# Optimization experiments

Hardware: AMD Instinct MI355X
Metric: run time of the kernel (lower is better)

The kernel has to match this reference:

```python
import jax, jax.numpy as jnp
import numpy as np
import math

B, S, D, H = 2, 2048, 1024, 16
DK = D // H


def setup_inputs() -> dict:
    key = jax.random.key(0)
    ks = jax.random.split(key, 14)
    inp = {
        "query": jax.random.normal(ks[0], (B, S, D), dtype=jnp.float32),
        "key": jax.random.normal(ks[1], (B, S, D), dtype=jnp.float32),
        "value": jax.random.normal(ks[2], (B, S, D), dtype=jnp.float32),
        "group_prob": jax.random.uniform(ks[3], (B, S, S), dtype=jnp.float32),
        "mask": jax.random.randint(ks[4], (B, S), 0, 2, dtype=jnp.int32),
    }
    scale = 0.02
    inp["Wq"] = jax.random.normal(ks[5], (D, D), dtype=jnp.float32) * scale
    inp["bq"] = jnp.zeros((D,), dtype=jnp.float32)
    inp["Wk"] = jax.random.normal(ks[6], (D, D), dtype=jnp.float32) * scale
    inp["bk"] = jnp.zeros((D,), dtype=jnp.float32)
    inp["Wv"] = jax.random.normal(ks[7], (D, D), dtype=jnp.float32) * scale
    inp["bv"] = jnp.zeros((D,), dtype=jnp.float32)
    inp["Wo"] = jax.random.normal(ks[8], (D, D), dtype=jnp.float32) * scale
    inp["bo"] = jnp.zeros((D,), dtype=jnp.float32)
    return inp


def reference(query, key, value, group_prob, mask, Wq, bq, Wk, bk, Wv, bv, Wo, bo):
    b, s, d = query.shape
    # project and split heads: [B,S,D] -> [B,H,S,DK]
    def proj(x, W, bias):
        return (x @ W.T + bias).reshape(b, s, H, DK).transpose(0, 2, 1, 3)

    q = proj(query, Wq, bq)
    k = proj(key, Wk, bk)
    v = proj(value, Wv, bv)

    scores = jnp.einsum("bhqd,bhkd->bhqk", q, k) / math.sqrt(DK)  # [B,H,S,S]

    # combined mask: padding-row mask OR diagonal (always attend to self)
    eye = jnp.eye(s, dtype=jnp.int32)
    combined = mask[:, None, None, :] | eye[None, None, :, :]  # [B,1,S,S]
    scores = jnp.where(combined == 0, jnp.float32(-1e9), scores)

    p_attn = jax.nn.softmax(scores, axis=-1)
    p_attn = p_attn * group_prob[:, None, :, :]  # post-softmax group scaling

    x = jnp.einsum("bhqk,bhkd->bhqd", p_attn, v)  # [B,H,S,DK]
    x = x.transpose(0, 2, 1, 3).reshape(b, s, d)
    return x @ Wo.T + bo
```

## Files before the change

### kernel.cpp

```cpp
#include <hip/hip_runtime.h>
#include <hip/hip_bf16.h>
#include <stdint.h>

typedef __bf16 bf16x8 __attribute__((ext_vector_type(8)));
typedef float f32x4 __attribute__((ext_vector_type(4)));

#define QSCALE 0.1803368801111244f

__device__ __forceinline__ void gld16(const void* g, void* l) {
  __builtin_amdgcn_global_load_lds(
      (__attribute__((address_space(1))) void*)(uintptr_t)(g),
      (__attribute__((address_space(3))) void*)(l), 16, 0, 0);
}

struct CastArgs {
  const float* src[7];
  __bf16* dst[7];
  int n[7];
};

__global__ __launch_bounds__(256) void cast_bf16_kernel(CastArgs a) {
  const int t = blockIdx.y;
  const int i = (blockIdx.x * 256 + threadIdx.x) * 8;
  if (i >= a.n[t]) return;
  const float4* s = (const float4*)(a.src[t] + i);
  float4 v0 = s[0], v1 = s[1];
  bf16x8 o;
  o[0] = (__bf16)v0.x; o[1] = (__bf16)v0.y; o[2] = (__bf16)v0.z; o[3] = (__bf16)v0.w;
  o[4] = (__bf16)v1.x; o[5] = (__bf16)v1.y; o[6] = (__bf16)v1.z; o[7] = (__bf16)v1.w;
  *(bf16x8*)(a.dst[t] + i) = o;
}

struct QkvArgs {
  const __bf16* A[3];
  const __bf16* B[3];
  const float* bias[3];
  __bf16* out[3];
};

__global__ __launch_bounds__(256) void qkv_gemm(QkvArgs args) {
  __shared__ __align__(16) __bf16 As[128 * 32];
  __shared__ __align__(16) __bf16 Bs[128 * 32];
  const int tid = threadIdx.x;
  const int z = blockIdx.y;
  const int bx = blockIdx.x;
  const int m0 = (z < 2 ? (bx >> 3) : (bx & 7)) * 128;
  const int n0 = (z < 2 ? (bx & 7) : (bx >> 3)) * 128;
  const __bf16* A = args.A[z];
  const __bf16* B = args.B[z];
  const float* bias = args.bias[z];
  __bf16* out = args.out[z];
  const float scale = (z == 0) ? QSCALE : 1.0f;

  const int lane = tid & 63, wid = tid >> 6;
  const int wm = (wid & 1) * 64, wn = (wid >> 1) * 64;
  const int l16 = lane & 15, quad = lane >> 4;

  const int sc = (tid & 3) ^ ((tid >> 2) & 3);
  const __bf16* ga = A + (size_t)(m0 + (tid >> 2)) * 1024 + sc * 8;
  const __bf16* gb = B + (size_t)(n0 + (tid >> 2)) * 1024 + sc * 8;
  char* lA = (char*)As + tid * 16;
  char* lB = (char*)Bs + tid * 16;
  const int a_off = (wm + l16) * 64 + ((quad ^ (l16 & 3)) * 16);
  const int b_off = (wn + l16) * 64 + ((quad ^ (l16 & 3)) * 16);

  f32x4 acc[4][4] = {};

  for (int k0 = 0; k0 < 1024; k0 += 32) {
    __syncthreads();
    gld16(ga + k0, lA);
    gld16(ga + k0 + 64 * 1024, lA + 4096);
    gld16(gb + k0, lB);
    gld16(gb + k0 + 64 * 1024, lB + 4096);
    __syncthreads();
    bf16x8 af[4], bfr[4];
#pragma unroll
    for (int mi = 0; mi < 4; ++mi)
      af[mi] = *(const bf16x8*)((const char*)As + a_off + mi * 1024);
#pragma unroll
    for (int ni = 0; ni < 4; ++ni)
      bfr[ni] = *(const bf16x8*)((const char*)Bs + b_off + ni * 1024);
#pragma unroll
    for (int mi = 0; mi < 4; ++mi)
#pragma unroll
      for (int ni = 0; ni < 4; ++ni)
        acc[mi][ni] = __builtin_amdgcn_mfma_f32_16x16x32_bf16(af[mi], bfr[ni],
                                                              acc[mi][ni], 0, 0, 0);
  }

  if (z < 2) {
#pragma unroll
    for (int ni = 0; ni < 4; ++ni) {
      const int col = n0 + wn + ni * 16 + l16;
      const int h = col >> 6, dk = col & 63;
      const float bb = bias[col];
#pragma unroll
      for (int mi = 0; mi < 4; ++mi)
#pragma unroll
        for (int r = 0; r < 4; ++r) {
          const int row = m0 + wm + mi * 16 + quad * 4 + r;
          const int b = row >> 11, s = row & 2047;
          out[((size_t)(b * 16 + h) * 2048 + s) * 64 + dk] =
              (__bf16)((acc[mi][ni][r] + bb) * scale);
        }
    }
  } else {
#pragma unroll
    for (int mi = 0; mi < 4; ++mi)
#pragma unroll
      for (int r = 0; r < 4; ++r) {
        const int rowm = m0 + wm + mi * 16 + quad * 4 + r;
        const int h = rowm >> 6, dk = rowm & 63;
        const float bb = bias[rowm];
#pragma unroll
        for (int ni = 0; ni < 4; ++ni) {
          const int coln = n0 + wn + ni * 16 + l16;
          const int b = coln >> 11, s = coln & 2047;
          out[((size_t)(b * 16 + h) * 64 + dk) * 2048 + s] =
              (__bf16)(acc[mi][ni][r] + bb);
        }
      }
  }
}

__global__ __launch_bounds__(256) void gemm_out(const __bf16* __restrict__ A,
                                                const __bf16* __restrict__ B,
                                                const float* __restrict__ bias,
                                                float* __restrict__ out) {
  __shared__ __align__(16) __bf16 As[128 * 32];
  __shared__ __align__(16) __bf16 Bs[128 * 32];
  const int tid = threadIdx.x;
  const int m0 = blockIdx.y * 128;
  const int n0 = blockIdx.x * 128;
  const int lane = tid & 63, wid = tid >> 6;
  const int wm = (wid & 1) * 64, wn = (wid >> 1) * 64;
  const int l16 = lane & 15, quad = lane >> 4;

  const int sc = (tid & 3) ^ ((tid >> 2) & 3);
  const __bf16* ga = A + (size_t)(m0 + (tid >> 2)) * 1024 + sc * 8;
  const __bf16* gb = B + (size_t)(n0 + (tid >> 2)) * 1024 + sc * 8;
  char* lA = (char*)As + tid * 16;
  char* lB = (char*)Bs + tid * 16;
  const int a_off = (wm + l16) * 64 + ((quad ^ (l16 & 3)) * 16);
  const int b_off = (wn + l16) * 64 + ((quad ^ (l16 & 3)) * 16);

  f32x4 acc[4][4] = {};

  for (int k0 = 0; k0 < 1024; k0 += 32) {
    __syncthreads();
    gld16(ga + k0, lA);
    gld16(ga + k0 + 64 * 1024, lA + 4096);
    gld16(gb + k0, lB);
    gld16(gb + k0 + 64 * 1024, lB + 4096);
    __syncthreads();
    bf16x8 af[4], bfr[4];
#pragma unroll
    for (int mi = 0; mi < 4; ++mi)
      af[mi] = *(const bf16x8*)((const char*)As + a_off + mi * 1024);
#pragma unroll
    for (int ni = 0; ni < 4; ++ni)
      bfr[ni] = *(const bf16x8*)((const char*)Bs + b_off + ni * 1024);
#pragma unroll
    for (int mi = 0; mi < 4; ++mi)
#pragma unroll
      for (int ni = 0; ni < 4; ++ni)
        acc[mi][ni] = __builtin_amdgcn_mfma_f32_16x16x32_bf16(af[mi], bfr[ni],
                                                              acc[mi][ni], 0, 0, 0);
  }

#pragma unroll
  for (int ni = 0; ni < 4; ++ni) {
    const int col = n0 + wn + ni * 16 + l16;
    const float bb = bias[col];
#pragma unroll
    for (int mi = 0; mi < 4; ++mi)
#pragma unroll
      for (int r = 0; r < 4; ++r) {
        const int row = m0 + wm + mi * 16 + quad * 4 + r;
        out[(size_t)row * 1024 + col] = acc[mi][ni][r] + bb;
      }
  }
}

__global__ __launch_bounds__(256) void attn_kernel(
    const __bf16* __restrict__ Qh, const __bf16* __restrict__ Kh,
    const __bf16* __restrict__ Vt, const float* __restrict__ gprob,
    const int* __restrict__ maskp, __bf16* __restrict__ xb) {
  __shared__ __align__(16) __bf16 Qs[64 * 64];
  __shared__ __align__(16) __bf16 Ks[2][64 * 64];
  __shared__ __align__(16) __bf16 Vs[2][64 * 64];
  __shared__ __align__(16) __bf16 Ps[4][16 * 64];
  __shared__ unsigned long long mbits[32];

  const int tid = threadIdx.x;
  const int qt = blockIdx.x, bh = blockIdx.y;
  const int b = bh >> 4, h = bh & 15;
  const int q0 = qt * 64;
  const int lane = tid & 63, wid = tid >> 6, l16 = lane & 15, quad = lane >> 4;
  const size_t head_off = (size_t)bh * (2048 * 64);

  const int srow = tid >> 3;
  const int sc8 = (tid & 7) ^ (srow & 7);
  const int fxor = (l16 & 7);

  const __bf16* gk0 = Kh + head_off + (size_t)srow * 64 + sc8 * 8;
  const __bf16* gv0 = Vt + head_off + (size_t)srow * 2048 + sc8 * 8;

  {
    const __bf16* gq = Qh + head_off + (size_t)(q0 + srow) * 64 + sc8 * 8;
    gld16(gq, (char*)Qs + tid * 16);
    gld16(gq + 32 * 64, (char*)Qs + 4096 + tid * 16);
    gld16(gk0, (char*)Ks + tid * 16);
    gld16(gk0 + 2048, (char*)Ks + 4096 + tid * 16);
    gld16(gv0, (char*)Vs + tid * 16);
    gld16(gv0 + 32 * 2048, (char*)Vs + 4096 + tid * 16);
  }
  {
    const int* mr = maskp + b * 2048;
#pragma unroll
    for (int t = 0; t < 8; ++t) {
      const int kt2 = wid * 8 + t;
      const int mv = mr[kt2 * 64 + lane];
      const unsigned long long bal = __ballot(mv != 0);
      if (lane == 0) mbits[kt2] = bal;
    }
  }
  __syncthreads();
  bf16x8 aq[2];
  aq[0] = *(const bf16x8*)((const char*)Qs + (wid * 16 + l16) * 128 +
                           ((quad ^ fxor) * 16));
  aq[1] = *(const bf16x8*)((const char*)Qs + (wid * 16 + l16) * 128 +
                           (((4 + quad) ^ fxor) * 16));

  f32x4 o[4] = {};
  float lp[4] = {0.f, 0.f, 0.f, 0.f};
  int irow[4];
#pragma unroll
  for (int r = 0; r < 4; ++r) irow[r] = q0 + wid * 16 + quad * 4 + r;

  const float* gpl = gprob + (size_t)b * 2048 * 2048 +
                     (size_t)(q0 + wid * 16 + l16) * 2048 + quad * 8;
  float4 g0 = *(const float4*)(gpl);
  float4 g1 = *(const float4*)(gpl + 4);
  float4 g2 = *(const float4*)(gpl + 32);
  float4 g3 = *(const float4*)(gpl + 36);

  for (int kt = 0; kt < 32; ++kt) {
    const int cur = kt & 1;
    float4 gn0, gn1, gn2, gn3;
    if (kt < 31) {
      const int nb = cur ^ 1;
      gld16(gk0 + (kt + 1) * 4096, (char*)Ks + nb * 8192 + tid * 16);
      gld16(gk0 + (kt + 1) * 4096 + 2048, (char*)Ks + nb * 8192 + 4096 + tid * 16);
      gld16(gv0 + (kt + 1) * 64, (char*)Vs + nb * 8192 + tid * 16);
      gld16(gv0 + (kt + 1) * 64 + 32 * 2048, (char*)Vs + nb * 8192 + 4096 + tid * 16);
      const float* gn = gpl + (kt + 1) * 64;
      gn0 = *(const float4*)(gn);
      gn1 = *(const float4*)(gn + 4);
      gn2 = *(const float4*)(gn + 32);
      gn3 = *(const float4*)(gn + 36);
    }

    const unsigned long long sh = mbits[kt] >> l16;
    const uint32_t shlo = (uint32_t)sh, shhi = (uint32_t)(sh >> 32);
    const bool mk[4] = {(shlo & 1) != 0, (shlo & 0x10000u) != 0,
                        (shhi & 1) != 0, (shhi & 0x10000u) != 0};

    f32x4 sc[4] = {};
#pragma unroll
    for (int kh = 0; kh < 2; ++kh)
#pragma unroll
      for (int ni = 0; ni < 4; ++ni) {
        bf16x8 bk = *(const bf16x8*)((const char*)Ks + cur * 8192 +
                                     (ni * 16 + l16) * 128 +
                                     (((kh * 4 + quad) ^ fxor) * 16));
        sc[ni] = __builtin_amdgcn_mfma_f32_16x16x32_bf16(aq[kh], bk, sc[ni], 0, 0, 0);
      }

    float pw[4][4];
    if (kt != qt) {
#pragma unroll
      for (int ni = 0; ni < 4; ++ni)
#pragma unroll
        for (int r = 0; r < 4; ++r) {
          const float e = __builtin_exp2f(sc[ni][r]);
          const float p = mk[ni] ? e : 0.f;
          lp[r] += p;
          pw[ni][r] = p;
        }
    } else {
#pragma unroll
      for (int ni = 0; ni < 4; ++ni)
#pragma unroll
        for (int r = 0; r < 4; ++r) {
          const float e = __builtin_exp2f(sc[ni][r]);
          const bool diag = (ni == wid) && (l16 == quad * 4 + r);
          const float p = (mk[ni] || diag) ? e : 0.f;
          lp[r] += p;
          pw[ni][r] = p;
        }
    }

#pragma unroll
    for (int ni = 0; ni < 4; ++ni)
#pragma unroll
      for (int r = 0; r < 4; ++r) {
        const int prow = quad * 4 + r;
        const int pchunk = (ni * 2 + (l16 >> 3)) ^ (prow & 7);
        *(__bf16*)((char*)&Ps[wid][0] + prow * 128 + pchunk * 16 + (l16 & 7) * 2) =
            (__bf16)pw[ni][r];
      }
    asm volatile("s_waitcnt lgkmcnt(0)" ::: "memory");

    const float gfl[16] = {g0.x, g0.y, g0.z, g0.w, g1.x, g1.y, g1.z, g1.w,
                           g2.x, g2.y, g2.z, g2.w, g3.x, g3.y, g3.z, g3.w};
#pragma unroll
    for (int kh = 0; kh < 2; ++kh) {
      bf16x8 ap = *(const bf16x8*)((const char*)&Ps[wid][0] + l16 * 128 +
                                   (((kh * 4 + quad) ^ fxor) * 16));
      bf16x8 apg;
#pragma unroll
      for (int j = 0; j < 8; ++j)
        apg[j] = (__bf16)((float)ap[j] * gfl[kh * 8 + j]);
#pragma unroll
      for (int ni = 0; ni < 4; ++ni) {
        bf16x8 bv = *(const bf16x8*)((const char*)Vs + cur * 8192 +
                                     (ni * 16 + l16) * 128 +
                                     (((kh * 4 + quad) ^ fxor) * 16));
        o[ni] = __builtin_amdgcn_mfma_f32_16x16x32_bf16(apg, bv, o[ni], 0, 0, 0);
      }
    }

    if (kt < 31) { g0 = gn0; g1 = gn1; g2 = gn2; g3 = gn3; }
    __syncthreads();
  }

#pragma unroll
  for (int r = 0; r < 4; ++r) {
    lp[r] += __shfl_xor(lp[r], 1);
    lp[r] += __shfl_xor(lp[r], 2);
    lp[r] += __shfl_xor(lp[r], 4);
    lp[r] += __shfl_xor(lp[r], 8);
    lp[r] = 1.f / lp[r];
  }
#pragma unroll
  for (int ni = 0; ni < 4; ++ni) {
    const int dk = ni * 16 + l16;
#pragma unroll
    for (int r = 0; r < 4; ++r) {
      const float val = o[ni][r] * lp[r];
      xb[((size_t)(b * 2048 + irow[r])) * 1024 + h * 64 + dk] = (__bf16)val;
    }
  }
}

extern "C" void kernel_launch(void* const* d_in, const int* in_sizes, int n_in,
                              void* d_out, int out_size, void* d_ws, size_t ws_size,
                              hipStream_t stream) {
  const float* query = (const float*)d_in[0];
  const float* key_  = (const float*)d_in[1];
  const float* value = (const float*)d_in[2];
  const float* gprob = (const float*)d_in[3];
  const int*   maskp = (const int*)d_in[4];
  const float* Wq = (const float*)d_in[5];
  const float* bq = (const float*)d_in[6];
  const float* Wk = (const float*)d_in[7];
  const float* bk = (const float*)d_in[8];
  const float* Wv = (const float*)d_in[9];
  const float* bv = (const float*)d_in[10];
  const float* Wo = (const float*)d_in[11];
  const float* bo = (const float*)d_in[12];

  char* ws = (char*)d_ws;
  const size_t MB = 1 << 20;
  __bf16* qb  = (__bf16*)(ws + 0 * MB);
  __bf16* kb  = (__bf16*)(ws + 8 * MB);
  __bf16* vb  = (__bf16*)(ws + 16 * MB);
  __bf16* Wqb = (__bf16*)(ws + 24 * MB);
  __bf16* Wkb = (__bf16*)(ws + 26 * MB);
  __bf16* Wvb = (__bf16*)(ws + 28 * MB);
  __bf16* Wob = (__bf16*)(ws + 30 * MB);
  __bf16* Qh  = (__bf16*)(ws + 32 * MB);
  __bf16* Kh  = (__bf16*)(ws + 40 * MB);
  __bf16* Vt  = (__bf16*)(ws + 48 * MB);
  __bf16* xb  = (__bf16*)(ws + 56 * MB);

  CastArgs ca;
  ca.src[0] = query; ca.dst[0] = qb;  ca.n[0] = 4194304;
  ca.src[1] = key_;  ca.dst[1] = kb;  ca.n[1] = 4194304;
  ca.src[2] = value; ca.dst[2] = vb;  ca.n[2] = 4194304;
  ca.src[3] = Wq;    ca.dst[3] = Wqb; ca.n[3] = 1048576;
  ca.src[4] = Wk;    ca.dst[4] = Wkb; ca.n[4] = 1048576;
  ca.src[5] = Wv;    ca.dst[5] = Wvb; ca.n[5] = 1048576;
  ca.src[6] = Wo;    ca.dst[6] = Wob; ca.n[6] = 1048576;
  cast_bf16_kernel<<<dim3(2048, 7), 256, 0, stream>>>(ca);

  QkvArgs qa;
  qa.A[0] = qb;  qa.B[0] = Wqb; qa.bias[0] = bq; qa.out[0] = Qh;
  qa.A[1] = kb;  qa.B[1] = Wkb; qa.bias[1] = bk; qa.out[1] = Kh;
  qa.A[2] = Wvb; qa.B[2] = vb;  qa.bias[2] = bv; qa.out[2] = Vt;
  qkv_gemm<<<dim3(256, 3), 256, 0, stream>>>(qa);

  attn_kernel<<<dim3(32, 32), 256, 0, stream>>>(Qh, Kh, Vt, gprob, maskp, xb);
  gemm_out<<<dim3(8, 32), 256, 0, stream>>>(xb, Wob, bo, (float*)d_out);
}
```

Before: 324.5 us.

## Cut attention LDS footprint, load Q into registers, remap blocks, fold group_prob early

The attention kernel now loads its Q fragments straight from global memory into registers, dropping the Qs buffer. It writes the P tile into the current K buffer after a barrier, dropping the Ps buffer, which shrinks shared memory and sets launch bounds for 4 blocks per CU. The group_prob factor is now loaded in the MFMA accumulator layout and multiplied in fp32 before the bf16 conversion, replacing a per-element bf16 unpack, multiply and repack. The grid is flattened and remapped so consecutive blocks spread across heads, which is meant to improve L2/XCD locality. The trade-offs are an extra barrier per iteration, and scalar uncoalesced gprob loads (16 per thread per tile) instead of float4 loads.

```diff
diff --git a/kernel.cpp b/kernel.cpp
--- a/kernel.cpp
+++ b/kernel.cpp
@@ -182,18 +182,19 @@
   }
 }
 
-__global__ __launch_bounds__(256) void attn_kernel(
+__global__ __launch_bounds__(256, 4) void attn_kernel(
     const __bf16* __restrict__ Qh, const __bf16* __restrict__ Kh,
     const __bf16* __restrict__ Vt, const float* __restrict__ gprob,
     const int* __restrict__ maskp, __bf16* __restrict__ xb) {
-  __shared__ __align__(16) __bf16 Qs[64 * 64];
   __shared__ __align__(16) __bf16 Ks[2][64 * 64];
   __shared__ __align__(16) __bf16 Vs[2][64 * 64];
-  __shared__ __align__(16) __bf16 Ps[4][16 * 64];
   __shared__ unsigned long long mbits[32];
 
   const int tid = threadIdx.x;
-  const int qt = blockIdx.x, bh = blockIdx.y;
+  const int flat = blockIdx.x;
+  const int ix = flat >> 3;
+  const int bh = (flat & 7) * 4 + (ix >> 5);
+  const int qt = ix & 31;
   const int b = bh >> 4, h = bh & 15;
   const int q0 = qt * 64;
   const int lane = tid & 63, wid = tid >> 6, l16 = lane & 15, quad = lane >> 4;
@@ -206,15 +207,33 @@
   const __bf16* gk0 = Kh + head_off + (size_t)srow * 64 + sc8 * 8;
   const __bf16* gv0 = Vt + head_off + (size_t)srow * 2048 + sc8 * 8;
 
+  gld16(gk0, (char*)Ks + tid * 16);
+  gld16(gk0 + 2048, (char*)Ks + 4096 + tid * 16);
+  gld16(gv0, (char*)Vs + tid * 16);
+  gld16(gv0 + 32 * 2048, (char*)Vs + 4096 + tid * 16);
+
+  bf16x8 aq[2];
   {
-    const __bf16* gq = Qh + head_off + (size_t)(q0 + srow) * 64 + sc8 * 8;
-    gld16(gq, (char*)Qs + tid * 16);
-    gld16(gq + 32 * 64, (char*)Qs + 4096 + tid * 16);
-    gld16(gk0, (char*)Ks + tid * 16);
-    gld16(gk0 + 2048, (char*)Ks + 4096 + tid * 16);
-    gld16(gv0, (char*)Vs + tid * 16);
-    gld16(gv0 + 32 * 2048, (char*)Vs + 4096 + tid * 16);
-  }
+    const __bf16* gq = Qh + head_off + (size_t)(q0 + wid * 16 + l16) * 64 + quad * 8;
+    aq[0] = *(const bf16x8*)(gq);
+    aq[1] = *(const bf16x8*)(gq + 32);
+  }
+
+  int irow[4];
+#pragma unroll
+  for (int r = 0; r < 4; ++r) irow[r] = q0 + wid * 16 + quad * 4 + r;
+
+  const float* gr[4];
+#pragma unroll
+  for (int r = 0; r < 4; ++r)
+    gr[r] = gprob + (size_t)b * 2048 * 2048 + (size_t)irow[r] * 2048 + l16;
+
+  float gc[4][4], gn[4][4];
+#pragma unroll
+  for (int ni = 0; ni < 4; ++ni)
+#pragma unroll
+    for (int r = 0; r < 4; ++r) gc[ni][r] = gr[r][ni * 16];
+
   {
     const int* mr = maskp + b * 2048;
 #pragma unroll
@@ -226,39 +245,23 @@
     }
   }
   __syncthreads();
-  bf16x8 aq[2];
-  aq[0] = *(const bf16x8*)((const char*)Qs + (wid * 16 + l16) * 128 +
-                           ((quad ^ fxor) * 16));
-  aq[1] = *(const bf16x8*)((const char*)Qs + (wid * 16 + l16) * 128 +
-                           (((4 + quad) ^ fxor) * 16));
 
   f32x4 o[4] = {};
   float lp[4] = {0.f, 0.f, 0.f, 0.f};
-  int irow[4];
-#pragma unroll
-  for (int r = 0; r < 4; ++r) irow[r] = q0 + wid * 16 + quad * 4 + r;
-
-  const float* gpl = gprob + (size_t)b * 2048 * 2048 +
-                     (size_t)(q0 + wid * 16 + l16) * 2048 + quad * 8;
-  float4 g0 = *(const float4*)(gpl);
-  float4 g1 = *(const float4*)(gpl + 4);
-  float4 g2 = *(const float4*)(gpl + 32);
-  float4 g3 = *(const float4*)(gpl + 36);
 
   for (int kt = 0; kt < 32; ++kt) {
     const int cur = kt & 1;
-    float4 gn0, gn1, gn2, gn3;
     if (kt < 31) {
       const int nb = cur ^ 1;
       gld16(gk0 + (kt + 1) * 4096, (char*)Ks + nb * 8192 + tid * 16);
       gld16(gk0 + (kt + 1) * 4096 + 2048, (char*)Ks + nb * 8192 + 4096 + tid * 16);
       gld16(gv0 + (kt + 1) * 64, (char*)Vs + nb * 8192 + tid * 16);
       gld16(gv0 + (kt + 1) * 64 + 32 * 2048, (char*)Vs + nb * 8192 + 4096 + tid * 16);
-      const float* gn = gpl + (kt + 1) * 64;
-      gn0 = *(const float4*)(gn);
-      gn1 = *(const float4*)(gn + 4);
-      gn2 = *(const float4*)(gn + 32);
-      gn3 = *(const float4*)(gn + 36);
+#pragma unroll
+      for (int ni = 0; ni < 4; ++ni)
+#pragma unroll
+        for (int r = 0; r < 4; ++r)
+          gn[ni][r] = gr[r][(kt + 1) * 64 + ni * 16];
     }
 
     const unsigned long long sh = mbits[kt] >> l16;
@@ -284,9 +287,9 @@
 #pragma unroll
         for (int r = 0; r < 4; ++r) {
           const float e = __builtin_exp2f(sc[ni][r]);
-          const float p = mk[ni] ? e : 0.f;
-          lp[r] += p;
-          pw[ni][r] = p;
+          const float em = mk[ni] ? e : 0.f;
+          lp[r] += em;
+          pw[ni][r] = em * gc[ni][r];
         }
     } else {
 #pragma unroll
@@ -295,43 +298,46 @@
         for (int r = 0; r < 4; ++r) {
           const float e = __builtin_exp2f(sc[ni][r]);
           const bool diag = (ni == wid) && (l16 == quad * 4 + r);
-          const float p = (mk[ni] || diag) ? e : 0.f;
-          lp[r] += p;
-          pw[ni][r] = p;
+          const float em = (mk[ni] || diag) ? e : 0.f;
+          lp[r] += em;
+          pw[ni][r] = em * gc[ni][r];
         }
     }
 
+    asm volatile("s_waitcnt lgkmcnt(0)\n\ts_barrier" ::: "memory");
+    __builtin_amdgcn_sched_barrier(0);
+
+    char* psw = (char*)Ks + cur * 8192 + wid * 2048;
 #pragma unroll
     for (int ni = 0; ni < 4; ++ni)
 #pragma unroll
       for (int r = 0; r < 4; ++r) {
         const int prow = quad * 4 + r;
         const int pchunk = (ni * 2 + (l16 >> 3)) ^ (prow & 7);
-        *(__bf16*)((char*)&Ps[wid][0] + prow * 128 + pchunk * 16 + (l16 & 7) * 2) =
+        *(__bf16*)(psw + prow * 128 + pchunk * 16 + (l16 & 7) * 2) =
             (__bf16)pw[ni][r];
       }
     asm volatile("s_waitcnt lgkmcnt(0)" ::: "memory");
-
-    const float gfl[16] = {g0.x, g0.y, g0.z, g0.w, g1.x, g1.y, g1.z, g1.w,
-                           g2.x, g2.y, g2.z, g2.w, g3.x, g3.y, g3.z, g3.w};
+    __builtin_amdgcn_sched_barrier(0);
+
 #pragma unroll
     for (int kh = 0; kh < 2; ++kh) {
-      bf16x8 ap = *(const bf16x8*)((const char*)&Ps[wid][0] + l16 * 128 +
-                                   (((kh * 4 + quad) ^ fxor) * 16));
-      bf16x8 apg;
-#pragma unroll
-      for (int j = 0; j < 8; ++j)
-        apg[j] = (__bf16)((float)ap[j] * gfl[kh * 8 + j]);
+      bf16x8 ap = *(const bf16x8*)(psw + l16 * 128 + (((kh * 4 + quad) ^ fxor) * 16));
 #pragma unroll
       for (int ni = 0; ni < 4; ++ni) {
         bf16x8 bv = *(const bf16x8*)((const char*)Vs + cur * 8192 +
                                      (ni * 16 + l16) * 128 +
                                      (((kh * 4 + quad) ^ fxor) * 16));
-        o[ni] = __builtin_amdgcn_mfma_f32_16x16x32_bf16(apg, bv, o[ni], 0, 0, 0);
+        o[ni] = __builtin_amdgcn_mfma_f32_16x16x32_bf16(ap, bv, o[ni], 0, 0, 0);
       }
     }
 
-    if (kt < 31) { g0 = gn0; g1 = gn1; g2 = gn2; g3 = gn3; }
+    if (kt < 31) {
+#pragma unroll
+      for (int ni = 0; ni < 4; ++ni)
+#pragma unroll
+        for (int r = 0; r < 4; ++r) gc[ni][r] = gn[ni][r];
+    }
     __syncthreads();
   }
 
@@ -401,6 +407,6 @@
   qa.A[2] = Wvb; qa.B[2] = vb;  qa.bias[2] = bv; qa.out[2] = Vt;
   qkv_gemm<<<dim3(256, 3), 256, 0, stream>>>(qa);
 
-  attn_kernel<<<dim3(32, 32), 256, 0, stream>>>(Qh, Kh, Vt, gprob, maskp, xb);
+  attn_kernel<<<dim3(1024), 256, 0, stream>>>(Qh, Kh, Vt, gprob, maskp, xb);
   gemm_out<<<dim3(8, 32), 256, 0, stream>>>(xb, Wob, bo, (float*)d_out);
 }
```

Measured after the change: 362.8 us. 1.12x slower.
